# Performance work log

Hardware: AMD Instinct MI355X
Metric: run time of the kernel (lower is better)

## Reference

```python
import jax, jax.numpy as jnp
import numpy as np

LOSS_WEIGHT = 1.0
STRIDE = 4.0
KEY_W = 0.5
BETA = 1.0 / STRIDE
BOUND2 = 1000.0 ** 2
TIME = 10


def _smooth_l1(pred, target):
    diff = jnp.abs(pred - target)
    return jnp.where(diff < BETA, 0.5 * diff * diff / BETA, diff - 0.5 * BETA)


def _interpolate(poly):
    # poly: (N, P, 2) -> (N, P*TIME, 2), linear interp between each pt and its roll-by-1 neighbor
    N, P, _ = poly.shape
    roll = jnp.roll(poly, shift=1, axis=1)
    step = jnp.arange(TIME, dtype=poly.dtype) / TIME          # (TIME,)
    interp = poly[:, :, None, :] * step[None, None, :, None] \
           + roll[:, :, None, :] * (1.0 - step)[None, None, :, None]  # (N,P,TIME,2)
    return interp.reshape(N, P * TIME, 2)


def _pairwise_sqdist(a, b):
    # matches compute_distance(pred_poly=a, gt_poly=b): out[n, j, i] = ||a[n,i] - b[n,j]||^2
    return jnp.sum((a[:, None, :, :] - b[:, :, None, :]) ** 2, axis=-1)  # (N, Mb, Ma)


def _masked_mean(loss, mask):
    # mean over selected (K, 2) elements, i.e. sum / (count*2)
    cnt = jnp.sum(mask.astype(loss.dtype)) * 2.0
    return jnp.sum(loss * mask[..., None].astype(loss.dtype)) / jnp.maximum(cnt, 1.0)


def setup_inputs() -> dict:
    key = jax.random.key(0)
    k1, k2, k3, k4, k5 = jax.random.split(key, 5)
    N, P = 256, 128
    return {
        "pred_contours": jax.random.normal(k1, (N, P, 2), jnp.float32),
        "pred_offsets": jax.random.normal(k2, (N, P, 2), jnp.float32),
        "gt_contours": jax.random.normal(k3, (N, P, 2), jnp.float32),
        "gt_key_points": jax.random.normal(k4, (N, P, 2), jnp.float32),
        "gt_key_points_mask": jax.random.randint(k5, (N, P), 0, 2, jnp.int32),
    }


def reference(pred_contours, pred_offsets, gt_contours, gt_key_points, gt_key_points_mask):
    masks = gt_key_points_mask.astype(bool)

    # ---- item 1: each pred point matched to nearest interpolated gt point ----
    targets = _interpolate(gt_contours)                       # (N, P*TIME, 2)
    d1 = _pairwise_sqdist(pred_contours, targets)             # (N, P*TIME, P)
    matched1 = jnp.min(d1, axis=1)                            # (N, P)
    idx_gt = jnp.argmin(d1, axis=1)                           # (N, P)
    valid1 = matched1 <= BOUND2
    tgt = jnp.take_along_axis(targets, idx_gt[..., None], axis=1)  # (N, P, 2)
    off_t1 = jax.lax.stop_gradient((tgt - pred_contours) / STRIDE)
    loss1 = _masked_mean(_smooth_l1(pred_offsets, off_t1), valid1) * (1.0 - KEY_W)

    # ---- item 2: each gt key point matched to nearest pred point ----
    d2 = _pairwise_sqdist(gt_key_points, pred_contours)       # (N, Ppred, Pkey)
    matched2 = jnp.min(d2, axis=1)                            # (N, Pkey)
    idx_pred = jnp.argmin(d2, axis=1)                         # (N, Pkey)
    valid2 = (matched2 <= BOUND2) & masks
    preds_g = jnp.take_along_axis(pred_contours, idx_pred[..., None], axis=1)
    offs_g = jnp.take_along_axis(pred_offsets, idx_pred[..., None], axis=1)
    off_t2 = jax.lax.stop_gradient((gt_key_points - preds_g) / STRIDE)
    loss2 = _masked_mean(_smooth_l1(offs_g, off_t2), valid2) * KEY_W

    return (loss1 + loss2) * LOSS_WEIGHT
```

## Files before the change

### kernel.cpp

```cpp
#include <hip/hip_runtime.h>


constexpr int N_  = 256;
constexpr int P_  = 128;
constexpr int T_  = 10;
constexpr int PT_ = P_ * T_;

__device__ __forceinline__ float smooth_l1(float diff) {
  float a = fabsf(diff);
  return (a < 0.25f) ? (2.0f * a * a) : (a - 0.125f);
}

__global__ __launch_bounds__(256) void dm_partial_kernel(
    const float* __restrict__ pred_c, const float* __restrict__ pred_o,
    const float* __restrict__ gt_c,  const float* __restrict__ gt_k,
    const int* __restrict__ mask, float4* __restrict__ partial)
{
  const int n    = blockIdx.x;
  const int tid  = threadIdx.x;
  const int i    = tid & (P_ - 1);
  const int half = tid >> 7;

  __shared__ float2 tg[PT_];
  __shared__ float2 pc[P_];
  __shared__ float2 po[P_];
  __shared__ float2 gc[P_];
  __shared__ float  bd[P_];
  __shared__ int    bi[P_];
  __shared__ float4 redv[4];

  const float2* pc_g = (const float2*)pred_c + n * P_;
  const float2* po_g = (const float2*)pred_o + n * P_;
  const float2* gc_g = (const float2*)gt_c  + n * P_;
  const float2* gk_g = (const float2*)gt_k  + n * P_;

  if (tid < P_) {
    pc[tid] = pc_g[tid];
    po[tid] = po_g[tid];
    gc[tid] = gc_g[tid];
  }
  __syncthreads();

  for (int j = tid; j < PT_; j += 256) {
    int p = j / T_;
    int t = j - p * T_;
    float s  = (float)t / 10.0f;
    float ns = 1.0f - s;
    float2 a = gc[p];
    float2 b = gc[(p + P_ - 1) & (P_ - 1)];
    float2 v;
    v.x = a.x * s + b.x * ns;
    v.y = a.y * s + b.y * ns;
    tg[j] = v;
  }
  __syncthreads();

  const float2 p = pc[i];
  float best = 3.0e38f; int bestj = 0;
  {
    const int j0 = half * (PT_ / 2);
    for (int j = j0; j < j0 + PT_ / 2; ++j) {
      float2 t = tg[j];
      float dx = p.x - t.x, dy = p.y - t.y;
      float d = dx * dx + dy * dy;
      if (d < best) { best = d; bestj = j; }
    }
  }
  if (half == 0) { bd[i] = best; bi[i] = bestj; }
  __syncthreads();
  if (half == 1 && best < bd[i]) { bd[i] = best; bi[i] = bestj; }
  __syncthreads();

  float s1 = 0.0f, c1 = 0.0f;
  if (half == 0) {
    float d = bd[i];
    if (d <= 1.0e6f) {
      float2 t = tg[bi[i]];
      float2 o = po[i];
      float tx = (t.x - p.x) * 0.25f;
      float ty = (t.y - p.y) * 0.25f;
      s1 = smooth_l1(o.x - tx) + smooth_l1(o.y - ty);
      c1 = 1.0f;
    }
  }
  __syncthreads();

  const float2 k = gk_g[i];
  float best2 = 3.0e38f; int bestj2 = 0;
  {
    const int j0 = half * (P_ / 2);
    for (int j = j0; j < j0 + P_ / 2; ++j) {
      float2 q = pc[j];
      float dx = k.x - q.x, dy = k.y - q.y;
      float d = dx * dx + dy * dy;
      if (d < best2) { best2 = d; bestj2 = j; }
    }
  }
  if (half == 0) { bd[i] = best2; bi[i] = bestj2; }
  __syncthreads();
  if (half == 1 && best2 < bd[i]) { bd[i] = best2; bi[i] = bestj2; }
  __syncthreads();

  float s2 = 0.0f, c2 = 0.0f;
  if (half == 0) {
    float d = bd[i];
    if (d <= 1.0e6f && mask[n * P_ + i] != 0) {
      int j = bi[i];
      float2 q = pc[j];
      float2 o = po[j];
      float tx = (k.x - q.x) * 0.25f;
      float ty = (k.y - q.y) * 0.25f;
      s2 = smooth_l1(o.x - tx) + smooth_l1(o.y - ty);
      c2 = 1.0f;
    }
  }

  #pragma unroll
  for (int off = 32; off > 0; off >>= 1) {
    s1 += __shfl_down(s1, off);
    c1 += __shfl_down(c1, off);
    s2 += __shfl_down(s2, off);
    c2 += __shfl_down(c2, off);
  }
  const int wave = tid >> 6;
  const int lane = tid & 63;
  if (lane == 0) redv[wave] = make_float4(s1, c1, s2, c2);
  __syncthreads();
  if (tid == 0) {
    float4 r = redv[0];
    #pragma unroll
    for (int w = 1; w < 4; ++w) {
      float4 q = redv[w];
      r.x += q.x; r.y += q.y; r.z += q.z; r.w += q.w;
    }
    partial[n] = r;
  }
}

__global__ __launch_bounds__(256) void dm_final_kernel(
    const float4* __restrict__ partial, float* __restrict__ out)
{
  const int tid = threadIdx.x;
  float4 v = partial[tid];
  float s1 = v.x, c1 = v.y, s2 = v.z, c2 = v.w;
  #pragma unroll
  for (int off = 32; off > 0; off >>= 1) {
    s1 += __shfl_down(s1, off);
    c1 += __shfl_down(c1, off);
    s2 += __shfl_down(s2, off);
    c2 += __shfl_down(c2, off);
  }
  __shared__ float4 redv[4];
  const int wave = tid >> 6;
  const int lane = tid & 63;
  if (lane == 0) redv[wave] = make_float4(s1, c1, s2, c2);
  __syncthreads();
  if (tid == 0) {
    float4 r = redv[0];
    #pragma unroll
    for (int w = 1; w < 4; ++w) {
      float4 q = redv[w];
      r.x += q.x; r.y += q.y; r.z += q.z; r.w += q.w;
    }
    float l1 = (r.x / fmaxf(r.y * 2.0f, 1.0f)) * 0.5f;
    float l2 = (r.z / fmaxf(r.w * 2.0f, 1.0f)) * 0.5f;
    out[0] = l1 + l2;
  }
}

extern "C" void kernel_launch(void* const* d_in, const int* in_sizes, int n_in,
                              void* d_out, int out_size, void* d_ws, size_t ws_size,
                              hipStream_t stream) {
  const float* pred_c = (const float*)d_in[0];
  const float* pred_o = (const float*)d_in[1];
  const float* gt_c   = (const float*)d_in[2];
  const float* gt_k   = (const float*)d_in[3];
  const int*   mask   = (const int*)d_in[4];
  float4* partial = (float4*)d_ws;

  dm_partial_kernel<<<N_, 256, 0, stream>>>(pred_c, pred_o, gt_c, gt_k, mask, partial);
  dm_final_kernel<<<1, 256, 0, stream>>>(partial, (float*)d_out);
}
```

Before: 79.08 us.

## Replace dense interpolated-point search with per-segment projection and wider blocks

Instead of materialising all ten interpolated points per gt segment and scanning them, each pred point projects onto every segment analytically and evaluates only the two neighbouring interpolation samples. This cuts the nearest-neighbour work roughly fivefold. Blocks grow to 1024 threads, splitting both searches across eight groups and merging through shared memory. Tie-breaking and floating-point rounding of the projection could pick a different index than an exhaustive argmin in near-degenerate cases.

```diff
diff --git a/kernel.cpp b/kernel.cpp
--- a/kernel.cpp
+++ b/kernel.cpp
@@ -1,33 +1,33 @@
 #include <hip/hip_runtime.h>
 
 
-constexpr int N_  = 256;
-constexpr int P_  = 128;
-constexpr int T_  = 10;
-constexpr int PT_ = P_ * T_;
+constexpr int N_ = 256;
+constexpr int P_ = 128;
 
 __device__ __forceinline__ float smooth_l1(float diff) {
   float a = fabsf(diff);
   return (a < 0.25f) ? (2.0f * a * a) : (a - 0.125f);
 }
 
-__global__ __launch_bounds__(256) void dm_partial_kernel(
+__global__ __launch_bounds__(1024) void dm_partial_kernel(
     const float* __restrict__ pred_c, const float* __restrict__ pred_o,
     const float* __restrict__ gt_c,  const float* __restrict__ gt_k,
     const int* __restrict__ mask, float4* __restrict__ partial)
 {
-  const int n    = blockIdx.x;
-  const int tid  = threadIdx.x;
-  const int i    = tid & (P_ - 1);
-  const int half = tid >> 7;
-
-  __shared__ float2 tg[PT_];
+  const int n   = blockIdx.x;
+  const int tid = threadIdx.x;
+  const int i   = tid & (P_ - 1);
+  const int q   = tid >> 7;
+
   __shared__ float2 pc[P_];
   __shared__ float2 po[P_];
-  __shared__ float2 gc[P_];
-  __shared__ float  bd[P_];
-  __shared__ int    bi[P_];
-  __shared__ float4 redv[4];
+  __shared__ float4 segA[P_];
+  __shared__ float2 segE[P_];
+  __shared__ float  segI[P_];
+  __shared__ float  st[12];
+  __shared__ float  bd[8][P_];
+  __shared__ int    bj[8][P_];
+  __shared__ float4 redw[16];
 
   const float2* pc_g = (const float2*)pred_c + n * P_;
   const float2* po_g = (const float2*)pred_o + n * P_;
@@ -35,50 +35,74 @@
   const float2* gk_g = (const float2*)gt_k  + n * P_;
 
   if (tid < P_) {
-    pc[tid] = pc_g[tid];
-    po[tid] = po_g[tid];
-    gc[tid] = gc_g[tid];
-  }
-  __syncthreads();
-
-  for (int j = tid; j < PT_; j += 256) {
-    int p = j / T_;
-    int t = j - p * T_;
-    float s  = (float)t / 10.0f;
-    float ns = 1.0f - s;
-    float2 a = gc[p];
-    float2 b = gc[(p + P_ - 1) & (P_ - 1)];
-    float2 v;
-    v.x = a.x * s + b.x * ns;
-    v.y = a.y * s + b.y * ns;
-    tg[j] = v;
-  }
-  __syncthreads();
-
-  const float2 p = pc[i];
+    int p = tid;
+    float2 a = gc_g[p];
+    float2 b = gc_g[(p + P_ - 1) & (P_ - 1)];
+    segA[p] = make_float4(a.x, a.y, b.x, b.y);
+    float ex = a.x - b.x, ey = a.y - b.y;
+    segE[p] = make_float2(ex, ey);
+    float e2 = ex * ex + ey * ey;
+    segI[p] = (e2 > 0.0f) ? (1.0f / e2) : 0.0f;
+  } else if (tid < 2 * P_) {
+    pc[tid - P_] = pc_g[tid - P_];
+  } else if (tid < 3 * P_) {
+    po[tid - 2 * P_] = po_g[tid - 2 * P_];
+  } else if (tid < 3 * P_ + 10) {
+    int t = tid - 3 * P_;
+    st[t] = (float)t / 10.0f;
+  }
+  __syncthreads();
+
+  const float2 pt = pc[i];
   float best = 3.0e38f; int bestj = 0;
   {
-    const int j0 = half * (PT_ / 2);
-    for (int j = j0; j < j0 + PT_ / 2; ++j) {
-      float2 t = tg[j];
-      float dx = p.x - t.x, dy = p.y - t.y;
-      float d = dx * dx + dy * dy;
-      if (d < best) { best = d; bestj = j; }
-    }
-  }
-  if (half == 0) { bd[i] = best; bi[i] = bestj; }
-  __syncthreads();
-  if (half == 1 && best < bd[i]) { bd[i] = best; bi[i] = bestj; }
+    const int p0 = q * 16;
+    #pragma unroll 4
+    for (int p = p0; p < p0 + 16; ++p) {
+      float4 ab  = segA[p];
+      float2 e   = segE[p];
+      float  inv = segI[p];
+      float fx = ab.z - pt.x, fy = ab.w - pt.y;
+      float ef = e.x * fx + e.y * fy;
+      float tf = -(ef * inv) * 10.0f;
+      int tl = (int)floorf(tf);
+      tl = min(max(tl, 0), 8);
+      float s0 = st[tl], s1v = st[tl + 1];
+      float ns0 = 1.0f - s0, ns1 = 1.0f - s1v;
+      float v0x = ab.x * s0 + ab.z * ns0;
+      float v0y = ab.y * s0 + ab.w * ns0;
+      float v1x = ab.x * s1v + ab.z * ns1;
+      float v1y = ab.y * s1v + ab.w * ns1;
+      float dx0 = pt.x - v0x, dy0 = pt.y - v0y;
+      float dx1 = pt.x - v1x, dy1 = pt.y - v1y;
+      float d0 = dx0 * dx0 + dy0 * dy0;
+      float d1 = dx1 * dx1 + dy1 * dy1;
+      bool c  = d1 < d0;
+      float dl = c ? d1 : d0;
+      int   jl = p * 10 + (c ? tl + 1 : tl);
+      if (dl < best) { best = dl; bestj = jl; }
+    }
+  }
+  bd[q][i] = best; bj[q][i] = bestj;
   __syncthreads();
 
   float s1 = 0.0f, c1 = 0.0f;
-  if (half == 0) {
-    float d = bd[i];
-    if (d <= 1.0e6f) {
-      float2 t = tg[bi[i]];
+  if (q == 0) {
+    float bb = bd[0][i]; int jj = bj[0][i];
+    #pragma unroll
+    for (int w = 1; w < 8; ++w) {
+      float d = bd[w][i];
+      if (d < bb) { bb = d; jj = bj[w][i]; }
+    }
+    if (bb <= 1.0e6f) {
+      int p = jj / 10, t = jj - (jj / 10) * 10;
+      float4 ab = segA[p];
+      float s  = st[t], ns = 1.0f - s;
+      float vx = ab.x * s + ab.z * ns;
+      float vy = ab.y * s + ab.w * ns;
       float2 o = po[i];
-      float tx = (t.x - p.x) * 0.25f;
-      float ty = (t.y - p.y) * 0.25f;
+      float tx = (vx - pt.x) * 0.25f;
+      float ty = (vy - pt.y) * 0.25f;
       s1 = smooth_l1(o.x - tx) + smooth_l1(o.y - ty);
       c1 = 1.0f;
     }
@@ -88,28 +112,31 @@
   const float2 k = gk_g[i];
   float best2 = 3.0e38f; int bestj2 = 0;
   {
-    const int j0 = half * (P_ / 2);
-    for (int j = j0; j < j0 + P_ / 2; ++j) {
-      float2 q = pc[j];
-      float dx = k.x - q.x, dy = k.y - q.y;
+    const int j0 = q * 16;
+    #pragma unroll 4
+    for (int j = j0; j < j0 + 16; ++j) {
+      float2 pp = pc[j];
+      float dx = k.x - pp.x, dy = k.y - pp.y;
       float d = dx * dx + dy * dy;
       if (d < best2) { best2 = d; bestj2 = j; }
     }
   }
-  if (half == 0) { bd[i] = best2; bi[i] = bestj2; }
-  __syncthreads();
-  if (half == 1 && best2 < bd[i]) { bd[i] = best2; bi[i] = bestj2; }
+  bd[q][i] = best2; bj[q][i] = bestj2;
   __syncthreads();
 
   float s2 = 0.0f, c2 = 0.0f;
-  if (half == 0) {
-    float d = bd[i];
-    if (d <= 1.0e6f && mask[n * P_ + i] != 0) {
-      int j = bi[i];
-      float2 q = pc[j];
-      float2 o = po[j];
-      float tx = (k.x - q.x) * 0.25f;
-      float ty = (k.y - q.y) * 0.25f;
+  if (q == 0) {
+    float bb = bd[0][i]; int jj = bj[0][i];
+    #pragma unroll
+    for (int w = 1; w < 8; ++w) {
+      float d = bd[w][i];
+      if (d < bb) { bb = d; jj = bj[w][i]; }
+    }
+    if (bb <= 1.0e6f && mask[n * P_ + i] != 0) {
+      float2 pp = pc[jj];
+      float2 o  = po[jj];
+      float tx = (k.x - pp.x) * 0.25f;
+      float ty = (k.y - pp.y) * 0.25f;
       s2 = smooth_l1(o.x - tx) + smooth_l1(o.y - ty);
       c2 = 1.0f;
     }
@@ -124,14 +151,14 @@
   }
   const int wave = tid >> 6;
   const int lane = tid & 63;
-  if (lane == 0) redv[wave] = make_float4(s1, c1, s2, c2);
+  if (lane == 0) redw[wave] = make_float4(s1, c1, s2, c2);
   __syncthreads();
   if (tid == 0) {
-    float4 r = redv[0];
-    #pragma unroll
-    for (int w = 1; w < 4; ++w) {
-      float4 q = redv[w];
-      r.x += q.x; r.y += q.y; r.z += q.z; r.w += q.w;
+    float4 r = redw[0];
+    #pragma unroll
+    for (int w = 1; w < 16; ++w) {
+      float4 v = redw[w];
+      r.x += v.x; r.y += v.y; r.z += v.z; r.w += v.w;
     }
     partial[n] = r;
   }
@@ -178,6 +205,6 @@
   const int*   mask   = (const int*)d_in[4];
   float4* partial = (float4*)d_ws;
 
-  dm_partial_kernel<<<N_, 256, 0, stream>>>(pred_c, pred_o, gt_c, gt_k, mask, partial);
+  dm_partial_kernel<<<N_, 1024, 0, stream>>>(pred_c, pred_o, gt_c, gt_k, mask, partial);
   dm_final_kernel<<<1, 256, 0, stream>>>(partial, (float*)d_out);
 }
```

Measured after the change: 70.18 us. 1.13x faster.
